# Kernel tuning notes

Hardware: AMD Instinct MI355X
Metric: run time of the kernel (lower is better)

Reference implementation:

```python
import jax, jax.numpy as jnp
import numpy as np
from jax import lax

KERNEL = 21
SHIFT = KERNEL - 1  # 20
NUM_LEVELS = 2
EPS = 1e-5
NEG_SLOPE = 0.01


def _conv1d(x, w):
    # x: [B, Cin, T], w: [Cout, Cin, K] -> [B, Cout, T-K+1]
    return lax.conv_general_dilated(x, w, window_strides=(1,), padding='VALID',
                                    dimension_numbers=('NCH', 'OIH', 'NCH'))


def _batchnorm_train(x, gamma, beta):
    # training-mode BN over (N, L) per channel, biased variance (torch semantics)
    mean = jnp.mean(x, axis=(0, 2), keepdims=True)
    var = jnp.mean((x - mean) ** 2, axis=(0, 2), keepdims=True)
    return (x - mean) * lax.rsqrt(var + EPS) * gamma[None, :, None] + beta[None, :, None]


def _spp(y, L, num_levels, pool):
    # y: [B, C, Tc]; L: [B] valid lengths. Level i has 2^i bins:
    #   bin j covers [j*floor(L/2^i), j*floor(L/2^i)+ceil(L/2^i)), matching
    #   F.max_pool1d/avg_pool1d(kernel=ceil(f), stride=floor(f)) on x[:, :, :L].
    B, C, Tc = y.shape
    pos = jnp.arange(Tc)[None, :]                     # [1, Tc]
    Lf = L.astype(jnp.float32)
    outs = []
    for i in range(num_levels):
        k = 2 ** i
        f = Lf / k
        stride = jnp.floor(f).astype(jnp.int32)        # [B]
        kern = jnp.ceil(f).astype(jnp.int32)           # [B]
        bins = []
        for j in range(k):
            start = j * stride                         # [B]
            mask = (pos >= start[:, None]) & (pos < (start + kern)[:, None])  # [B, Tc]
            m = mask[:, None, :]                       # [B, 1, Tc]
            if pool == 'max':
                bins.append(jnp.max(jnp.where(m, y, -jnp.inf), axis=-1))      # [B, C]
            else:
                s = jnp.sum(jnp.where(m, y, jnp.zeros((), y.dtype)), axis=-1)
                bins.append(s / kern[:, None].astype(y.dtype))
        # torch .view flattens (C, k) channel-major
        outs.append(jnp.stack(bins, axis=-1).reshape(B, C * k))
    return jnp.concatenate(outs, axis=1)               # [B, C*(2^n - 1)]


def setup_inputs() -> dict:
    key = jax.random.key(0)
    k1, k2, k3, k4, k5 = jax.random.split(key, 5)
    B, C, T = 32, 64, 16384
    n_tasks = 2
    n_lin = 2 * C * (2 ** NUM_LEVELS - 1)  # 384
    x = jax.random.normal(k1, (B, C, T), dtype=jnp.float32)
    orig_len = jax.random.randint(k2, (B,), T // 2, T + 1, dtype=jnp.int32)
    w1 = jax.random.normal(k3, (C, C, KERNEL), dtype=jnp.float32) * 0.05
    w2 = jax.random.normal(k4, (C, C, KERNEL), dtype=jnp.float32) * 0.05
    g1 = jnp.ones((C,), jnp.float32); b1 = jnp.zeros((C,), jnp.float32)
    g2 = jnp.ones((C,), jnp.float32); b2 = jnp.zeros((C,), jnp.float32)
    fc_w = jax.random.normal(k5, (n_tasks, n_lin), dtype=jnp.float32) * 0.05
    fc_b = jnp.zeros((n_tasks,), jnp.float32)
    return {"x": x, "orig_len": orig_len, "w1": w1, "g1": g1, "b1": b1,
            "w2": w2, "g2": g2, "b2": b2, "fc_w": fc_w, "fc_b": fc_b}


def reference(x, orig_len, w1, g1, b1, w2, g2, b2, fc_w, fc_b):
    L = orig_len - SHIFT  # valid conv-output length per sample
    y1 = jax.nn.leaky_relu(_batchnorm_train(_conv1d(x, w1), g1, b1), NEG_SLOPE)
    p1 = _spp(y1, L, NUM_LEVELS, 'max')
    y2 = jax.nn.leaky_relu(_batchnorm_train(_conv1d(x, w2), g2, b2), NEG_SLOPE)
    p2 = _spp(y2, L, NUM_LEVELS, 'avg')
    feat = jnp.concatenate([p1, p2], axis=1)           # [B, 384]
    return feat @ fc_w.T + fc_b
```

## Files before the change

kernel.cpp:

```cpp
#include <hip/hip_runtime.h>

#define AS1 __attribute__((address_space(1)))
#define AS3 __attribute__((address_space(3)))

using u16 = unsigned short;
using u32 = unsigned int;
typedef __attribute__((ext_vector_type(8))) short bf16x8;
typedef __attribute__((ext_vector_type(4))) float f32x4;

constexpr int Bn    = 32;
constexpr int Tn    = 16384;
constexpr int TCn   = 16364;
constexpr int TILE  = 256;
constexpr int XROWS = 280;
constexpr int TPAD  = 16416;
constexpr int SPPCH = 64;

__device__ __forceinline__ u16 f2bf(float f) {
  union { float f; u32 u; } v; v.f = f;
  u32 u = v.u;
  u += 0x7fffu + ((u >> 16) & 1u);
  return (u16)(u >> 16);
}
__device__ __forceinline__ float bf2f(u32 h) {
  union { u32 u; float f; } v; v.u = h << 16; return v.f;
}
__device__ __forceinline__ u32 encf(float f) {
  union { float f; u32 u; } v; v.f = f;
  return (v.u & 0x80000000u) ? ~v.u : (v.u | 0x80000000u);
}
__device__ __forceinline__ float decf(u32 u) {
  union { u32 u; float f; } v;
  v.u = (u & 0x80000000u) ? (u ^ 0x80000000u) : ~u;
  return v.f;
}
__device__ __forceinline__ void gload_lds16(const void* g, void* l) {
  __builtin_amdgcn_global_load_lds((const AS1 u32*)g, (AS3 u32*)l, 16, 0, 0);
}
__device__ __forceinline__ float leaky(float z) { return z > 0.f ? z : 0.01f * z; }

__global__ __launch_bounds__(256) void transpose_x(const float* __restrict__ x,
                                                   u16* __restrict__ x_t,
                                                   const float* __restrict__ w1,
                                                   const float* __restrict__ w2,
                                                   u16* __restrict__ wf1,
                                                   u16* __restrict__ wf2) {
  __shared__ u16 lt[64][64];
  const int bx  = blockIdx.x;
  const int tid = threadIdx.x;

  if (bx >= Bn * 256) {
    const int bxx = bx - Bn * 256;
    const int cv  = bxx / 42;
    const int c   = bxx % 42;
    const float* w = cv ? w2 : w1;
    u16* wf = cv ? wf2 : wf1;
    const int ct   = tid >> 6;
    const int lane = tid & 63;
    const int q  = lane >> 4;
    const int rr = lane & 15;
    const int k  = c >> 1;
    const int cb = (c & 1) * 32;
    const int co = ct * 16 + rr;
    u16 us[8] __attribute__((aligned(16)));
#pragma unroll
    for (int j = 0; j < 8; ++j) {
      int ci = cb + q * 8 + j;
      us[j] = f2bf(w[((size_t)co * 64 + ci) * 21 + k]);
    }
    *(uint4*)&wf[((size_t)(c * 4 + ct) * 64 + lane) * 8] = *(const uint4*)us;
    return;
  }

  const int b   = bx >> 8;
  const int tt  = bx & 255;
  const int t0  = tt * 64;
  const int ci0 = (tid & 15) * 4;
  const int tl0 = (tid >> 4) * 4;
  float4 v[4];
#pragma unroll
  for (int j = 0; j < 4; ++j)
    v[j] = *(const float4*)(x + (size_t)(b * 64 + ci0 + j) * Tn + t0 + tl0);
  float vr[4][4] = {{v[0].x,v[0].y,v[0].z,v[0].w},{v[1].x,v[1].y,v[1].z,v[1].w},
                    {v[2].x,v[2].y,v[2].z,v[2].w},{v[3].x,v[3].y,v[3].z,v[3].w}};
#pragma unroll
  for (int e = 0; e < 4; ++e) {
    int tl = tl0 + e;
    u32 lo = (u32)f2bf(vr[0][e]) | ((u32)f2bf(vr[1][e]) << 16);
    u32 hi = (u32)f2bf(vr[2][e]) | ((u32)f2bf(vr[3][e]) << 16);
    uint2 pk = make_uint2(lo, hi);
    *(uint2*)&lt[tl][ci0] = pk;
  }
  __syncthreads();
  const int row = tid >> 2;
  const int seg = tid & 3;
  const int c0  = seg * 16;
  const int sw  = (row & 7) * 8;
  u16* op = x_t + ((size_t)b * TPAD + t0 + row) * 64 + c0;
  *(uint4*)op       = *(const uint4*)&lt[row][c0 ^ sw];
  *(uint4*)(op + 8) = *(const uint4*)&lt[row][(c0 + 8) ^ sw];
  if (tt == 0) {
    uint4 z = make_uint4(0u, 0u, 0u, 0u);
    uint4* pz = (uint4*)(x_t + ((size_t)b * TPAD + Tn) * 64);
    pz[tid] = z;
  }
}

__global__ __launch_bounds__(256, 3) void conv_mfma(const u16* __restrict__ x_t,
                                                    const u16* __restrict__ wf1,
                                                    const u16* __restrict__ wf2,
                                                    u16* __restrict__ y1,
                                                    u16* __restrict__ y2,
                                                    float* __restrict__ stats) {
  __shared__ u16 xs[XROWS * 64];
  __shared__ float sred[128];

  const int bid  = blockIdx.x;
  const int cv   = bid & 1;
  const int tmp  = bid >> 1;
  const int tile = tmp & 63;
  const int b    = tmp >> 6;
  const int t0   = tile * TILE;
  const int tid  = threadIdx.x;
  const int w    = tid >> 6;
  const int lane = tid & 63;
  const int q    = lane >> 4;
  const int r    = lane & 15;
  const u16* wf  = cv ? wf2 : wf1;

  if (tid < 128) sred[tid] = 0.f;

  const u16* xg = x_t + ((size_t)b * TPAD + t0) * 64;
  for (int s = w; s < 35; s += 4)
    gload_lds16(xg + (size_t)s * 512 + lane * 8, &xs[s * 512]);

  const u16* wfl = wf + lane * 8;
  bf16x8 afA0[4], afB0[4], afA1[4], afB1[4];
#pragma unroll
  for (int ct = 0; ct < 4; ++ct) {
    afA0[ct] = *(const bf16x8*)(wfl + (size_t)0 * 2048 + ct * 512);
    afB0[ct] = *(const bf16x8*)(wfl + (size_t)1 * 2048 + ct * 512);
    afA1[ct] = *(const bf16x8*)(wfl + (size_t)2 * 2048 + ct * 512);
    afB1[ct] = *(const bf16x8*)(wfl + (size_t)3 * 2048 + ct * 512);
  }

  __syncthreads();

  f32x4 acc[4][4];
#pragma unroll
  for (int a = 0; a < 4; ++a)
#pragma unroll
    for (int t = 0; t < 4; ++t)
      acc[a][t] = (f32x4){0.f, 0.f, 0.f, 0.f};

  const int rowbase = w * 64 + r;

  auto phase = [&](const bf16x8 (&af)[4], int k, int cb) {
    const int swl = ((rowbase + k) & 7) * 8;
    const int cid = (cb + q * 8) ^ swl;
    bf16x8 bx[4];
#pragma unroll
    for (int tt = 0; tt < 4; ++tt)
      bx[tt] = *(const bf16x8*)&xs[(rowbase + tt * 16 + k) * 64 + cid];
    __builtin_amdgcn_s_setprio(1);
#pragma unroll
    for (int ct = 0; ct < 4; ++ct)
#pragma unroll
      for (int tt = 0; tt < 4; ++tt)
        acc[ct][tt] = __builtin_amdgcn_mfma_f32_16x16x32_bf16(af[ct], bx[tt], acc[ct][tt], 0, 0, 0);
    __builtin_amdgcn_s_setprio(0);
  };
  auto loadaf = [&](bf16x8 (&af)[4], int c) {
    const u16* p = wfl + (size_t)c * 2048;
#pragma unroll
    for (int ct = 0; ct < 4; ++ct) af[ct] = *(const bf16x8*)(p + ct * 512);
  };

  for (int ii = 0; ii < 10; ++ii) {
    const int k0 = 2 * ii, k1 = 2 * ii + 1;
    phase(afA0, k0, 0);  loadaf(afA0, 4 * ii + 4);
    phase(afB0, k0, 32); loadaf(afB0, 4 * ii + 5);
    phase(afA1, k1, 0);  if (ii < 9) loadaf(afA1, 4 * ii + 6);
    phase(afB1, k1, 32); if (ii < 9) loadaf(afB1, 4 * ii + 7);
  }
  phase(afA0, 20, 0);
  phase(afB0, 20, 32);

  const bool full_t = (t0 + TILE <= TCn);
#pragma unroll
  for (int ct = 0; ct < 4; ++ct)
#pragma unroll
    for (int i = 0; i < 4; ++i) {
      float sv = 0.f, sq = 0.f;
      if (full_t) {
#pragma unroll
        for (int tt = 0; tt < 4; ++tt) {
          float v = acc[ct][tt][i];
          sv += v; sq += v * v;
        }
      } else {
#pragma unroll
        for (int tt = 0; tt < 4; ++tt) {
          int tg = t0 + w * 64 + tt * 16 + r;
          if (tg < TCn) {
            float v = acc[ct][tt][i];
            sv += v; sq += v * v;
          }
        }
      }
#pragma unroll
      for (int m = 1; m < 16; m <<= 1) {
        sv += __shfl_xor(sv, m, 64);
        sq += __shfl_xor(sq, m, 64);
      }
      if (r == 0) {
        int co = ct * 16 + q * 4 + i;
        atomicAdd(&sred[co * 2], sv);
        atomicAdd(&sred[co * 2 + 1], sq);
      }
    }

  __syncthreads();

  u16* ys = xs;
#pragma unroll
  for (int ct = 0; ct < 4; ++ct)
#pragma unroll
    for (int tt = 0; tt < 4; ++tt) {
      int tl = w * 64 + tt * 16 + r;
      int sw = (tl & 7) * 8;
      int co0 = (ct * 16 + q * 4) ^ sw;
      u32 lo = (u32)f2bf(acc[ct][tt][0]) | ((u32)f2bf(acc[ct][tt][1]) << 16);
      u32 hi = (u32)f2bf(acc[ct][tt][2]) | ((u32)f2bf(acc[ct][tt][3]) << 16);
      *(uint2*)&ys[tl * 64 + co0] = make_uint2(lo, hi);
    }
  __syncthreads();
  u16* yo = (cv ? y2 : y1) + ((size_t)b * Tn + t0) * 64;
#pragma unroll
  for (int m = 0; m < 8; ++m) {
    int flat = m * 256 + tid;
    int row  = flat >> 3;
    int c0   = (flat & 7) * 8;
    int sw   = (row & 7) * 8;
    *(uint4*)(yo + (size_t)row * 64 + c0) = *(const uint4*)&ys[row * 64 + (c0 ^ sw)];
  }
  if (tid < 128) atomicAdd(&stats[cv * 128 + tid], sred[tid]);
}

__global__ __launch_bounds__(256) void spp(const u16* __restrict__ y1,
                                           const u16* __restrict__ y2,
                                           const float* __restrict__ stats,
                                           const float* __restrict__ g1v,
                                           const float* __restrict__ b1v,
                                           const float* __restrict__ g2v,
                                           const float* __restrict__ b2v,
                                           const int* __restrict__ orig_len,
                                           u32* __restrict__ part) {
  __shared__ float lred[4][16][4][5];
  const int bx = blockIdx.x;
  const int b  = bx >> 6;
  const int ch = bx & 63;
  const int tid  = threadIdx.x;
  const int g    = tid & 15;
  const int trow = tid >> 4;
  const int wv   = tid >> 6;
  const int co0  = g * 4;
  const int L     = orig_len[b] - 20;
  const int str2  = L >> 1;
  const int kern2 = L - str2;
  const float Nf = 32.0f * 16364.0f;
  float a1[4], c1[4], a2[4], c2[4];
#pragma unroll
  for (int j = 0; j < 4; ++j) {
    int co = co0 + j;
    float s, sq, mean, var;
    s = stats[co * 2]; sq = stats[co * 2 + 1];
    mean = s / Nf; var = sq / Nf - mean * mean; if (var < 0.f) var = 0.f;
    a1[j] = g1v[co] * rsqrtf(var + 1e-5f);
    c1[j] = b1v[co] - mean * a1[j];
    s = stats[128 + co * 2]; sq = stats[128 + co * 2 + 1];
    mean = s / Nf; var = sq / Nf - mean * mean; if (var < 0.f) var = 0.f;
    a2[j] = g2v[co] * rsqrtf(var + 1e-5f);
    c2[j] = b2v[co] - mean * a2[j];
  }
  float m1[4] = {-3.4e38f,-3.4e38f,-3.4e38f,-3.4e38f};
  float m2[4] = {-3.4e38f,-3.4e38f,-3.4e38f,-3.4e38f};
  float s0[4] = {0,0,0,0}, sb0[4] = {0,0,0,0}, sb1[4] = {0,0,0,0};
  const int tbase = ch * 256;
  int tend = tbase + 256;
  if (tend > L) tend = L;
  const u16* p1 = y1 + (size_t)b * Tn * 64 + co0;
  const u16* p2 = y2 + (size_t)b * Tn * 64 + co0;

  auto body = [&](int t) {
    uint2 v1 = *(const uint2*)(p1 + (size_t)t * 64);
    uint2 v2 = *(const uint2*)(p2 + (size_t)t * 64);
    float f1[4] = { bf2f(v1.x & 0xffffu), bf2f(v1.x >> 16),
                    bf2f(v1.y & 0xffffu), bf2f(v1.y >> 16) };
    float f2[4] = { bf2f(v2.x & 0xffffu), bf2f(v2.x >> 16),
                    bf2f(v2.y & 0xffffu), bf2f(v2.y >> 16) };
    bool in0 = (t < kern2), in1 = (t >= str2);
#pragma unroll
    for (int j = 0; j < 4; ++j) {
      float z1 = leaky(fmaf(a1[j], f1[j], c1[j]));
      float z2 = leaky(fmaf(a2[j], f2[j], c2[j]));
      s0[j] += z2;
      if (in0) { m1[j] = fmaxf(m1[j], z1); sb0[j] += z2; }
      if (in1) { m2[j] = fmaxf(m2[j], z1); sb1[j] += z2; }
    }
  };

  if (tend == tbase + 256) {
#pragma unroll 4
    for (int it = 0; it < 16; ++it)
      body(tbase + trow + it * 16);
  } else {
    for (int t = tbase + trow; t < tend; t += 16)
      body(t);
  }

#pragma unroll
  for (int m = 16; m <= 32; m <<= 1) {
#pragma unroll
    for (int j = 0; j < 4; ++j) {
      m1[j]  = fmaxf(m1[j], __shfl_xor(m1[j], m, 64));
      m2[j]  = fmaxf(m2[j], __shfl_xor(m2[j], m, 64));
      s0[j]  += __shfl_xor(s0[j],  m, 64);
      sb0[j] += __shfl_xor(sb0[j], m, 64);
      sb1[j] += __shfl_xor(sb1[j], m, 64);
    }
  }
  if (((tid & 63) >> 4) == 0) {
#pragma unroll
    for (int j = 0; j < 4; ++j) {
      lred[wv][g][j][0] = m1[j];
      lred[wv][g][j][1] = m2[j];
      lred[wv][g][j][2] = s0[j];
      lred[wv][g][j][3] = sb0[j];
      lred[wv][g][j][4] = sb1[j];
    }
  }
  __syncthreads();
  if (tid < 64) {
    const int co = tid;
    const int g2 = co >> 2, j2 = co & 3;
    float fm1 = lred[0][g2][j2][0], fm2 = lred[0][g2][j2][1];
    float fs0 = lred[0][g2][j2][2], fb0 = lred[0][g2][j2][3], fb1v_ = lred[0][g2][j2][4];
#pragma unroll
    for (int k = 1; k < 4; ++k) {
      fm1 = fmaxf(fm1, lred[k][g2][j2][0]);
      fm2 = fmaxf(fm2, lred[k][g2][j2][1]);
      fs0 += lred[k][g2][j2][2];
      fb0 += lred[k][g2][j2][3];
      fb1v_ += lred[k][g2][j2][4];
    }
    u32* pp = part + (size_t)bx * 384;
    float* pf = (float*)pp;
    u32 e1 = encf(fm1), e2 = encf(fm2);
    pp[co]              = e1 > e2 ? e1 : e2;
    pp[64 + co * 2]     = e1;
    pp[64 + co * 2 + 1] = e2;
    pf[192 + co]         = fs0;
    pf[256 + co * 2]     = fb0;
    pf[256 + co * 2 + 1] = fb1v_;
  }
}

__global__ __launch_bounds__(384) void fc(const u32* __restrict__ part,
                                          const int* __restrict__ orig_len,
                                          const float* __restrict__ fc_w,
                                          const float* __restrict__ fc_b,
                                          float* __restrict__ out) {
  __shared__ float r0s[6], r1s[6];
  const int b = blockIdx.x;
  const int j = threadIdx.x;
  const int L = orig_len[b] - 20;
  const int kern2 = L - (L >> 1);
  const u32* pb = part + (size_t)b * 64 * 384;
  float fv;
  if (j < 192) {
    u32 vmax = 0u;
    for (int c = 0; c < 64; ++c) {
      u32 v = pb[(size_t)c * 384 + j];
      vmax = v > vmax ? v : vmax;
    }
    fv = decf(vmax);
  } else {
    const float* pf = (const float*)pb;
    float s = 0.f;
    for (int c = 0; c < 64; ++c) s += pf[(size_t)c * 384 + j];
    fv = (j < 256) ? s / (float)L : s / (float)kern2;
  }
  float a0 = fv * fc_w[j];
  float a1 = fv * fc_w[384 + j];
#pragma unroll
  for (int m = 1; m < 64; m <<= 1) {
    a0 += __shfl_xor(a0, m, 64);
    a1 += __shfl_xor(a1, m, 64);
  }
  const int wv = j >> 6, ln = j & 63;
  if (ln == 0) { r0s[wv] = a0; r1s[wv] = a1; }
  __syncthreads();
  if (j == 0) {
    float t0 = 0.f, t1 = 0.f;
#pragma unroll
    for (int k = 0; k < 6; ++k) { t0 += r0s[k]; t1 += r1s[k]; }
    out[b * 2]     = t0 + fc_b[0];
    out[b * 2 + 1] = t1 + fc_b[1];
  }
}

extern "C" void kernel_launch(void* const* d_in, const int* in_sizes, int n_in,
                              void* d_out, int out_size, void* d_ws, size_t ws_size,
                              hipStream_t stream) {
  const float* x        = (const float*)d_in[0];
  const int*   orig_len = (const int*)d_in[1];
  const float* w1  = (const float*)d_in[2];
  const float* g1  = (const float*)d_in[3];
  const float* b1  = (const float*)d_in[4];
  const float* w2  = (const float*)d_in[5];
  const float* g2  = (const float*)d_in[6];
  const float* b2  = (const float*)d_in[7];
  const float* fcw = (const float*)d_in[8];
  const float* fcb = (const float*)d_in[9];
  float* out = (float*)d_out;

  char* ws = (char*)d_ws;
  const size_t XT_BYTES = (size_t)Bn * TPAD * 64 * 2;
  const size_t Y_BYTES  = (size_t)Bn * Tn * 64 * 2;
  const size_t WF_BYTES = (size_t)42 * 4 * 64 * 8 * 2;
  size_t off = 0;
  u16* x_t = (u16*)(ws + off); off += XT_BYTES;
  u16* y1  = (u16*)(ws + off); off += Y_BYTES;
  u16* y2  = (u16*)(ws + off); off += Y_BYTES;
  u16* wf1 = (u16*)(ws + off); off += WF_BYTES;
  u16* wf2 = (u16*)(ws + off); off += WF_BYTES;
  float* stats = (float*)(ws + off);
  u32*   part  = (u32*)(ws + off + 1024);

  hipMemsetAsync(stats, 0, 1024, stream);
  transpose_x<<<Bn * 256 + 84, 256, 0, stream>>>(x, x_t, w1, w2, wf1, wf2);
  conv_mfma<<<Bn * 64 * 2, 256, 0, stream>>>(x_t, wf1, wf2, y1, y2, stats);
  spp<<<Bn * SPPCH, 256, 0, stream>>>(y1, y2, stats, g1, b1, g2, b2, orig_len, part);
  fc<<<Bn, 384, 0, stream>>>(part, orig_len, fcw, fcb, out);
  (void)in_sizes; (void)n_in; (void)out_size; (void)ws_size;
}
```

Measured before the change: 390.0 us.

## Fuse input transpose and bf16 conversion into conv kernel load stage

Removes the separate transpose kernel that wrote a padded, channel-last bf16 copy of x to workspace. The conv kernel now reads fp32 x directly, converts it to bf16 and stores it transposed and XOR-swizzled into LDS, zero-filling rows past the end of the sequence. This removes a full write and re-read of the intermediate tensor and one launch. In exchange each conv block reads twice the bytes per element. Both conv-branch blocks and overlapping halo rows (320 staged rows per 256-row tile) re-read the same fp32 data, and the loads are now synchronous register loads instead of async direct-to-LDS loads.

```diff
diff --git a/kernel.cpp b/kernel.cpp
--- a/kernel.cpp
+++ b/kernel.cpp
@@ -12,8 +12,7 @@
 constexpr int Tn    = 16384;
 constexpr int TCn   = 16364;
 constexpr int TILE  = 256;
-constexpr int XROWS = 280;
-constexpr int TPAD  = 16416;
+constexpr int XSROWS = 320;
 constexpr int SPPCH = 64;
 
 __device__ __forceinline__ u16 f2bf(float f) {
@@ -34,85 +33,41 @@
   v.u = (u & 0x80000000u) ? (u ^ 0x80000000u) : ~u;
   return v.f;
 }
-__device__ __forceinline__ void gload_lds16(const void* g, void* l) {
-  __builtin_amdgcn_global_load_lds((const AS1 u32*)g, (AS3 u32*)l, 16, 0, 0);
-}
 __device__ __forceinline__ float leaky(float z) { return z > 0.f ? z : 0.01f * z; }
 
-__global__ __launch_bounds__(256) void transpose_x(const float* __restrict__ x,
-                                                   u16* __restrict__ x_t,
-                                                   const float* __restrict__ w1,
-                                                   const float* __restrict__ w2,
-                                                   u16* __restrict__ wf1,
-                                                   u16* __restrict__ wf2) {
-  __shared__ u16 lt[64][64];
-  const int bx  = blockIdx.x;
+__global__ __launch_bounds__(256) void wrepack(const float* __restrict__ w1,
+                                               const float* __restrict__ w2,
+                                               u16* __restrict__ wf1,
+                                               u16* __restrict__ wf2) {
+  const int bxx = blockIdx.x;
   const int tid = threadIdx.x;
-
-  if (bx >= Bn * 256) {
-    const int bxx = bx - Bn * 256;
-    const int cv  = bxx / 42;
-    const int c   = bxx % 42;
-    const float* w = cv ? w2 : w1;
-    u16* wf = cv ? wf2 : wf1;
-    const int ct   = tid >> 6;
-    const int lane = tid & 63;
-    const int q  = lane >> 4;
-    const int rr = lane & 15;
-    const int k  = c >> 1;
-    const int cb = (c & 1) * 32;
-    const int co = ct * 16 + rr;
-    u16 us[8] __attribute__((aligned(16)));
-#pragma unroll
-    for (int j = 0; j < 8; ++j) {
-      int ci = cb + q * 8 + j;
-      us[j] = f2bf(w[((size_t)co * 64 + ci) * 21 + k]);
-    }
-    *(uint4*)&wf[((size_t)(c * 4 + ct) * 64 + lane) * 8] = *(const uint4*)us;
-    return;
-  }
-
-  const int b   = bx >> 8;
-  const int tt  = bx & 255;
-  const int t0  = tt * 64;
-  const int ci0 = (tid & 15) * 4;
-  const int tl0 = (tid >> 4) * 4;
-  float4 v[4];
-#pragma unroll
-  for (int j = 0; j < 4; ++j)
-    v[j] = *(const float4*)(x + (size_t)(b * 64 + ci0 + j) * Tn + t0 + tl0);
-  float vr[4][4] = {{v[0].x,v[0].y,v[0].z,v[0].w},{v[1].x,v[1].y,v[1].z,v[1].w},
-                    {v[2].x,v[2].y,v[2].z,v[2].w},{v[3].x,v[3].y,v[3].z,v[3].w}};
-#pragma unroll
-  for (int e = 0; e < 4; ++e) {
-    int tl = tl0 + e;
-    u32 lo = (u32)f2bf(vr[0][e]) | ((u32)f2bf(vr[1][e]) << 16);
-    u32 hi = (u32)f2bf(vr[2][e]) | ((u32)f2bf(vr[3][e]) << 16);
-    uint2 pk = make_uint2(lo, hi);
-    *(uint2*)&lt[tl][ci0] = pk;
-  }
-  __syncthreads();
-  const int row = tid >> 2;
-  const int seg = tid & 3;
-  const int c0  = seg * 16;
-  const int sw  = (row & 7) * 8;
-  u16* op = x_t + ((size_t)b * TPAD + t0 + row) * 64 + c0;
-  *(uint4*)op       = *(const uint4*)&lt[row][c0 ^ sw];
-  *(uint4*)(op + 8) = *(const uint4*)&lt[row][(c0 + 8) ^ sw];
-  if (tt == 0) {
-    uint4 z = make_uint4(0u, 0u, 0u, 0u);
-    uint4* pz = (uint4*)(x_t + ((size_t)b * TPAD + Tn) * 64);
-    pz[tid] = z;
-  }
-}
-
-__global__ __launch_bounds__(256, 3) void conv_mfma(const u16* __restrict__ x_t,
+  const int cv  = bxx / 42;
+  const int c   = bxx % 42;
+  const float* w = cv ? w2 : w1;
+  u16* wf = cv ? wf2 : wf1;
+  const int ct   = tid >> 6;
+  const int lane = tid & 63;
+  const int q  = lane >> 4;
+  const int rr = lane & 15;
+  const int k  = c >> 1;
+  const int cb = (c & 1) * 32;
+  const int co = ct * 16 + rr;
+  u16 us[8] __attribute__((aligned(16)));
+#pragma unroll
+  for (int j = 0; j < 8; ++j) {
+    int ci = cb + q * 8 + j;
+    us[j] = f2bf(w[((size_t)co * 64 + ci) * 21 + k]);
+  }
+  *(uint4*)&wf[((size_t)(c * 4 + ct) * 64 + lane) * 8] = *(const uint4*)us;
+}
+
+__global__ __launch_bounds__(256, 3) void conv_mfma(const float* __restrict__ x,
                                                     const u16* __restrict__ wf1,
                                                     const u16* __restrict__ wf2,
                                                     u16* __restrict__ y1,
                                                     u16* __restrict__ y2,
                                                     float* __restrict__ stats) {
-  __shared__ u16 xs[XROWS * 64];
+  __shared__ u16 xs[XSROWS * 64];
   __shared__ float sred[128];
 
   const int bid  = blockIdx.x;
@@ -130,9 +85,34 @@
 
   if (tid < 128) sred[tid] = 0.f;
 
-  const u16* xg = x_t + ((size_t)b * TPAD + t0) * 64;
-  for (int s = w; s < 35; s += 4)
-    gload_lds16(xg + (size_t)s * 512 + lane * 8, &xs[s * 512]);
+  const float* xb = x + (size_t)b * 64 * Tn;
+  const int sci0 = (tid & 15) * 4;
+  const int stl0 = (tid >> 4) * 4;
+#pragma unroll
+  for (int p = 0; p < 5; ++p) {
+    const int row = p * 64 + stl0;
+    const int gt  = t0 + row;
+    float4 v0, v1, v2, v3;
+    if (gt < Tn) {
+      const float* pb0 = xb + (size_t)sci0 * Tn + gt;
+      v0 = *(const float4*)(pb0);
+      v1 = *(const float4*)(pb0 + Tn);
+      v2 = *(const float4*)(pb0 + 2 * Tn);
+      v3 = *(const float4*)(pb0 + 3 * Tn);
+    } else {
+      v0 = v1 = v2 = v3 = make_float4(0.f, 0.f, 0.f, 0.f);
+    }
+    const float vr[4][4] = {{v0.x,v0.y,v0.z,v0.w},{v1.x,v1.y,v1.z,v1.w},
+                            {v2.x,v2.y,v2.z,v2.w},{v3.x,v3.y,v3.z,v3.w}};
+#pragma unroll
+    for (int e = 0; e < 4; ++e) {
+      int rr2 = row + e;
+      int sw  = (rr2 & 7) * 8;
+      u32 lo = (u32)f2bf(vr[0][e]) | ((u32)f2bf(vr[1][e]) << 16);
+      u32 hi = (u32)f2bf(vr[2][e]) | ((u32)f2bf(vr[3][e]) << 16);
+      *(uint2*)&xs[rr2 * 64 + (sci0 ^ sw)] = make_uint2(lo, hi);
+    }
+  }
 
   const u16* wfl = wf + lane * 8;
   bf16x8 afA0[4], afB0[4], afA1[4], afB1[4];
@@ -426,11 +406,9 @@
   float* out = (float*)d_out;
 
   char* ws = (char*)d_ws;
-  const size_t XT_BYTES = (size_t)Bn * TPAD * 64 * 2;
   const size_t Y_BYTES  = (size_t)Bn * Tn * 64 * 2;
   const size_t WF_BYTES = (size_t)42 * 4 * 64 * 8 * 2;
   size_t off = 0;
-  u16* x_t = (u16*)(ws + off); off += XT_BYTES;
   u16* y1  = (u16*)(ws + off); off += Y_BYTES;
   u16* y2  = (u16*)(ws + off); off += Y_BYTES;
   u16* wf1 = (u16*)(ws + off); off += WF_BYTES;
@@ -439,8 +417,8 @@
   u32*   part  = (u32*)(ws + off + 1024);
 
   hipMemsetAsync(stats, 0, 1024, stream);
-  transpose_x<<<Bn * 256 + 84, 256, 0, stream>>>(x, x_t, w1, w2, wf1, wf2);
-  conv_mfma<<<Bn * 64 * 2, 256, 0, stream>>>(x_t, wf1, wf2, y1, y2, stats);
+  wrepack<<<84, 256, 0, stream>>>(w1, w2, wf1, wf2);
+  conv_mfma<<<Bn * 64 * 2, 256, 0, stream>>>(x, wf1, wf2, y1, y2, stats);
   spp<<<Bn * SPPCH, 256, 0, stream>>>(y1, y2, stats, g1, b1, g2, b2, orig_len, part);
   fc<<<Bn, 384, 0, stream>>>(part, orig_len, fcw, fcb, out);
   (void)in_sizes; (void)n_in; (void)out_size; (void)ws_size;
```

Result: no change. 389.7 us (-0.1%).
